# Kernel tuning notes

Measured on AMD Instinct MI355X. Metric: run time of the kernel, lower is better.

Reference implementation:

```python
import jax, jax.numpy as jnp
import numpy as np

N_NODES = 100000


def _add_self_loops(edges, n):
    loop = jnp.arange(n, dtype=edges.dtype)
    src = jnp.concatenate([edges[0], loop])
    dst = jnp.concatenate([edges[1], loop])
    return src, dst


def _gcn_conv(x, W, b, src, dst, dinv):
    # linear transform first (PyG GCNConv), then normalized scatter-add aggregation
    h = x @ W                                    # [N, out]
    norm = dinv[src] * dinv[dst]                 # [E]
    msg = h[src] * norm[:, None]                 # [E, out]
    out = jax.ops.segment_sum(msg, dst, num_segments=x.shape[0])
    return out + b


def setup_inputs() -> dict:
    key = jax.random.key(0)
    k1, k2, k3, k4 = jax.random.split(key, 4)
    feats, hidden, labels, n_edges = 128, 64, 16, 1600000
    features = jax.random.normal(k1, (N_NODES, feats), dtype=jnp.float32)
    edges = jax.random.randint(k2, (2, n_edges), 0, N_NODES, dtype=jnp.int64)
    W1 = jax.random.normal(k3, (feats, hidden), dtype=jnp.float32) * (1.0 / np.sqrt(feats))
    b1 = jnp.zeros((hidden,), dtype=jnp.float32)
    W2 = jax.random.normal(k4, (hidden, labels), dtype=jnp.float32) * (1.0 / np.sqrt(hidden))
    b2 = jnp.zeros((labels,), dtype=jnp.float32)
    return {"features": features, "edges": edges, "W1": W1, "b1": b1, "W2": W2, "b2": b2}


def reference(features, edges, W1, b1, W2, b2):
    n = features.shape[0]
    src, dst = _add_self_loops(edges, n)
    deg = jnp.zeros((n,), dtype=features.dtype).at[dst].add(1.0)  # in-degree incl. self loop
    dinv = jnp.where(deg > 0, jax.lax.rsqrt(deg), 0.0)
    h1 = jax.nn.relu(_gcn_conv(features, W1, b1, src, dst, dinv))
    h2 = _gcn_conv(h1, W2, b2, src, dst, dinv)
    return jax.nn.log_softmax(h2, axis=1)
```

## Files before the change

### kernel.cpp

```cpp
#include <hip/hip_runtime.h>
#include <math.h>

#define NN 100000
#define NE 1600000
#define FI 128
#define FH 64
#define FO 16
#define NB 392
#define BCAP 5632
#define AEPT 16
#define ACHUNK (256 * AEPT)
#define ABLK ((NE + ACHUNK - 1) / ACHUNK)
#define GBLK ((NN + 63) / 64)

typedef unsigned short ushort_t;
typedef __attribute__((ext_vector_type(8))) short bf16x8;
typedef __attribute__((ext_vector_type(4))) float f32x4;

__device__ __forceinline__ ushort_t f2bf(float f) {
    unsigned u = __float_as_uint(f);
    u = (u + 0x7fffu + ((u >> 16) & 1u)) >> 16;
    return (ushort_t)u;
}
__device__ __forceinline__ float bf_lo(unsigned u) {
    return __uint_as_float(u << 16);
}
__device__ __forceinline__ float bf_hi(unsigned u) {
    return __uint_as_float(u & 0xffff0000u);
}

__device__ __forceinline__ int load_dst(const int* edges, int mode, int e) {
    return mode ? edges[2 * (NE + e)] : edges[NE + e];
}
__device__ __forceinline__ int load_src(const int* edges, int mode, int e) {
    return mode ? edges[2 * e] : edges[e];
}

__global__ __launch_bounds__(256) void k_fuseA(const int* __restrict__ edges,
                                               unsigned* __restrict__ bcur,
                                               unsigned* __restrict__ staged,
                                               const float* __restrict__ x,
                                               const float* __restrict__ W1,
                                               ushort_t* __restrict__ h1p) {
    __shared__ unsigned pay_lds[ACHUNK];
    __shared__ ushort_t bkt_lds[ACHUNK];
    __shared__ unsigned hcnt[NB], hb[NB], dlt[NB], hcur[NB];
    __shared__ unsigned sc[512];
    __shared__ int smode;

    if (blockIdx.x >= ABLK) {
        const int tid = threadIdx.x;
        const int l = tid & 63;
        const int w = tid >> 6;
        const int m = l & 15;
        const int g = l >> 4;
        const int node0 = (blockIdx.x - ABLK) * 64 + w * 16;

        bf16x8 bfrag[4][4];
#pragma unroll
        for (int ks = 0; ks < 4; ++ks)
#pragma unroll
            for (int nt = 0; nt < 4; ++nt)
#pragma unroll
                for (int e = 0; e < 8; ++e)
                    bfrag[ks][nt][e] = (short)f2bf(W1[(ks * 32 + g * 8 + e) * FH + nt * 16 + m]);

        f32x4 acc[4];
#pragma unroll
        for (int nt = 0; nt < 4; ++nt) acc[nt] = (f32x4){0.f, 0.f, 0.f, 0.f};

        int node = node0 + m;
        const float* xrow = x + (size_t)(node < NN ? node : NN - 1) * FI;
#pragma unroll
        for (int ks = 0; ks < 4; ++ks) {
            float4 xa = *(const float4*)&xrow[ks * 32 + g * 8];
            float4 xb = *(const float4*)&xrow[ks * 32 + g * 8 + 4];
            bf16x8 afrag;
            afrag[0] = (short)f2bf(xa.x);
            afrag[1] = (short)f2bf(xa.y);
            afrag[2] = (short)f2bf(xa.z);
            afrag[3] = (short)f2bf(xa.w);
            afrag[4] = (short)f2bf(xb.x);
            afrag[5] = (short)f2bf(xb.y);
            afrag[6] = (short)f2bf(xb.z);
            afrag[7] = (short)f2bf(xb.w);
#pragma unroll
            for (int nt = 0; nt < 4; ++nt)
                acc[nt] = __builtin_amdgcn_mfma_f32_16x16x32_bf16(afrag, bfrag[ks][nt], acc[nt], 0, 0, 0);
        }
#pragma unroll
        for (int nt = 0; nt < 4; ++nt)
#pragma unroll
            for (int r = 0; r < 4; ++r) {
                int outnode = node0 + g * 4 + r;
                if (outnode < NN)
                    h1p[(size_t)outnode * FH + nt * 16 + m] = f2bf(acc[nt][r]);
            }
        return;
    }

    const int t = threadIdx.x;
    if (t == 0) {
        unsigned orv = 0;
        for (int i = 0; i < 16; ++i) orv |= (unsigned)edges[2 * i + 1];
        smode = (orv == 0u) ? 1 : 0;
    }
    for (int i = t; i < NB; i += 256) { hcnt[i] = 0; hcur[i] = 0; }
    __syncthreads();
    const int m = smode;
    const int base_e = blockIdx.x * ACHUNK;
    const int total = min(ACHUNK, NE - base_e);

    unsigned pay[AEPT];
    ushort_t bk[AEPT];
#pragma unroll
    for (int q = 0; q < AEPT; ++q) {
        int e = base_e + t + q * 256;
        pay[q] = 0;
        bk[q] = 0xffff;
        if (e < NE) {
            int d = load_dst(edges, m, e);
            int s = load_src(edges, m, e);
            pay[q] = ((unsigned)s << 8) | (unsigned)(d & 255);
            bk[q] = (ushort_t)(d >> 8);
            atomicAdd(&hcnt[d >> 8], 1u);
        }
    }
    __syncthreads();

    for (int i = t; i < NB; i += 256) dlt[i] = atomicAdd(&bcur[i], hcnt[i]);
    sc[t] = (t < NB) ? hcnt[t] : 0u;
    sc[t + 256] = (t + 256 < NB) ? hcnt[t + 256] : 0u;
    __syncthreads();
    for (int ofs = 1; ofs < 512; ofs <<= 1) {
        unsigned v0 = (t >= ofs) ? sc[t - ofs] : 0u;
        unsigned v1 = (t + 256 >= ofs) ? sc[t + 256 - ofs] : 0u;
        __syncthreads();
        sc[t] += v0;
        sc[t + 256] += v1;
        __syncthreads();
    }
    for (int i = t; i < NB; i += 256) hb[i] = sc[i] - hcnt[i];
    __syncthreads();
    for (int i = t; i < NB; i += 256) dlt[i] = dlt[i] - hb[i];
    __syncthreads();

#pragma unroll
    for (int q = 0; q < AEPT; ++q) {
        if (bk[q] != 0xffff) {
            unsigned b = bk[q];
            unsigned r = atomicAdd(&hcur[b], 1u);
            unsigned idx = hb[b] + r;
            pay_lds[idx] = pay[q];
            bkt_lds[idx] = (ushort_t)b;
        }
    }
    __syncthreads();

    for (int i = t; i < total; i += 256) {
        unsigned b = bkt_lds[i];
        unsigned within = (unsigned)i + dlt[b];
        if (within < BCAP)
            staged[(size_t)b * BCAP + within] = pay_lds[i];
    }
}

__global__ __launch_bounds__(256) void k_phaseB(const unsigned* __restrict__ staged,
                                                const unsigned* __restrict__ bcur,
                                                unsigned* __restrict__ rowstart,
                                                int* __restrict__ esrc,
                                                float* __restrict__ dinv) {
    __shared__ unsigned hist[256], hb[256], hcur[256], tmp[256];
    __shared__ unsigned sbc[512];
    const int b = blockIdx.x;
    const int t = threadIdx.x;

    sbc[t] = (t < NB) ? bcur[t] : 0u;
    sbc[t + 256] = (t + 256 < NB) ? bcur[t + 256] : 0u;
    __syncthreads();
    for (int ofs = 1; ofs < 512; ofs <<= 1) {
        unsigned v0 = (t >= ofs) ? sbc[t - ofs] : 0u;
        unsigned v1 = (t + 256 >= ofs) ? sbc[t + 256 - ofs] : 0u;
        __syncthreads();
        sbc[t] += v0;
        sbc[t + 256] += v1;
        __syncthreads();
    }
    const unsigned base = (b == 0) ? 0u : sbc[b - 1];
    const unsigned cnt = min(bcur[b], (unsigned)BCAP);

    hist[t] = 0;
    hcur[t] = 0;
    __syncthreads();
    const unsigned* sb = staged + (size_t)b * BCAP;
    for (unsigned i = t; i < cnt; i += 256) atomicAdd(&hist[sb[i] & 255u], 1u);
    __syncthreads();
    unsigned x = hist[t];
    tmp[t] = x;
    __syncthreads();
    for (int ofs = 1; ofs < 256; ofs <<= 1) {
        unsigned v = (t >= ofs) ? tmp[t - ofs] : 0u;
        __syncthreads();
        tmp[t] += v;
        __syncthreads();
    }
    hb[t] = tmp[t] - x;
    int v = b * 256 + t;
    if (v <= NN) rowstart[v] = base + hb[t];
    if (v < NN) dinv[v] = rsqrtf((float)(1u + x));
    __syncthreads();
    for (unsigned i = t; i < cnt; i += 256) {
        unsigned p = sb[i];
        unsigned dlo = p & 255u;
        unsigned pos = base + hb[dlo] + atomicAdd(&hcur[dlo], 1u);
        esrc[pos] = (int)(p >> 8);
    }
}

__global__ __launch_bounds__(256) void k_gather1f(const unsigned* __restrict__ rowstart,
                                                  const int* __restrict__ esrc,
                                                  const ushort_t* __restrict__ h1p,
                                                  const float* __restrict__ dinv,
                                                  const float* __restrict__ b1,
                                                  const float* __restrict__ W2,
                                                  ushort_t* __restrict__ h2p) {
    __shared__ float Ws2t[FO][FH];
    {
        int t = threadIdx.x;
#pragma unroll
        for (int i = 0; i < 4; ++i) {
            int q = t * 4 + i;
            int k = q >> 4, j = q & 15;
            Ws2t[j][k] = W2[q];
        }
    }
    __syncthreads();

    int wave = (blockIdx.x * 256 + threadIdx.x) >> 6;
    int lane = threadIdx.x & 63;
    int grp = lane >> 4;
    int fj = lane & 15;
    int v = wave * 4 + grp;
    if (v >= NN) return;

    const uint2* h2v = (const uint2*)h1p;
    unsigned beg = rowstart[v], end = rowstart[v + 1];
    float dv = dinv[v];
    float a0 = 0.f, a1 = 0.f, a2 = 0.f, a3 = 0.f;
    unsigned i = beg;
    int ns0 = 0, ns1 = 0, ns2 = 0, ns3 = 0;
    if (i + 3 < end) { ns0 = esrc[i]; ns1 = esrc[i + 1]; ns2 = esrc[i + 2]; ns3 = esrc[i + 3]; }
    while (i + 3 < end) {
        int s0 = ns0, s1 = ns1, s2 = ns2, s3 = ns3;
        unsigned nx = i + 4;
        if (nx + 3 < end) { ns0 = esrc[nx]; ns1 = esrc[nx + 1]; ns2 = esrc[nx + 2]; ns3 = esrc[nx + 3]; }
        float n0 = dinv[s0] * dv, n1 = dinv[s1] * dv;
        float n2 = dinv[s2] * dv, n3 = dinv[s3] * dv;
        uint2 u0 = h2v[(size_t)s0 * 16 + fj];
        uint2 u1 = h2v[(size_t)s1 * 16 + fj];
        uint2 u2 = h2v[(size_t)s2 * 16 + fj];
        uint2 u3 = h2v[(size_t)s3 * 16 + fj];
        a0 += bf_lo(u0.x) * n0 + bf_lo(u1.x) * n1 + bf_lo(u2.x) * n2 + bf_lo(u3.x) * n3;
        a1 += bf_hi(u0.x) * n0 + bf_hi(u1.x) * n1 + bf_hi(u2.x) * n2 + bf_hi(u3.x) * n3;
        a2 += bf_lo(u0.y) * n0 + bf_lo(u1.y) * n1 + bf_lo(u2.y) * n2 + bf_lo(u3.y) * n3;
        a3 += bf_hi(u0.y) * n0 + bf_hi(u1.y) * n1 + bf_hi(u2.y) * n2 + bf_hi(u3.y) * n3;
        i = nx;
    }
    for (; i < end; ++i) {
        int s = esrc[i];
        float n = dinv[s] * dv;
        uint2 u = h2v[(size_t)s * 16 + fj];
        a0 += bf_lo(u.x) * n;
        a1 += bf_hi(u.x) * n;
        a2 += bf_lo(u.y) * n;
        a3 += bf_hi(u.y) * n;
    }
    float di2 = dv * dv;
    uint2 us = h2v[(size_t)v * 16 + fj];
    float4 bb = ((const float4*)b1)[fj];
    float r0 = fmaxf(a0 + bf_lo(us.x) * di2 + bb.x, 0.f);
    float r1 = fmaxf(a1 + bf_hi(us.x) * di2 + bb.y, 0.f);
    float r2 = fmaxf(a2 + bf_lo(us.y) * di2 + bb.z, 0.f);
    float r3 = fmaxf(a3 + bf_hi(us.y) * di2 + bb.w, 0.f);

    float p[16];
#pragma unroll
    for (int j = 0; j < 16; ++j) {
        float4 w = *(const float4*)&Ws2t[j][fj * 4];
        p[j] = r0 * w.x + r1 * w.y + r2 * w.z + r3 * w.w;
    }
    bool c0 = (fj & 1) != 0;
    float q8[8];
#pragma unroll
    for (int k = 0; k < 8; ++k) {
        float sent = c0 ? p[2 * k] : p[2 * k + 1];
        float kept = c0 ? p[2 * k + 1] : p[2 * k];
        q8[k] = kept + __shfl_xor(sent, 1);
    }
    bool c1 = (fj & 2) != 0;
    float q4[4];
#pragma unroll
    for (int k = 0; k < 4; ++k) {
        float sent = c1 ? q8[2 * k] : q8[2 * k + 1];
        float kept = c1 ? q8[2 * k + 1] : q8[2 * k];
        q4[k] = kept + __shfl_xor(sent, 2);
    }
    bool c2 = (fj & 4) != 0;
    float q2[2];
#pragma unroll
    for (int k = 0; k < 2; ++k) {
        float sent = c2 ? q4[2 * k] : q4[2 * k + 1];
        float kept = c2 ? q4[2 * k + 1] : q4[2 * k];
        q2[k] = kept + __shfl_xor(sent, 4);
    }
    bool c3 = (fj & 8) != 0;
    {
        float sent = c3 ? q2[0] : q2[1];
        float kept = c3 ? q2[1] : q2[0];
        float fin = kept + __shfl_xor(sent, 8);
        h2p[(size_t)v * FO + fj] = f2bf(fin);
    }
}

__global__ __launch_bounds__(256) void k_gather2(const unsigned* __restrict__ rowstart,
                                                 const int* __restrict__ esrc,
                                                 const ushort_t* __restrict__ h2p,
                                                 const float* __restrict__ dinv,
                                                 const float* __restrict__ b,
                                                 float* __restrict__ out) {
    int wave = (blockIdx.x * 256 + threadIdx.x) >> 6;
    int lane = threadIdx.x & 63;
    int grp = lane >> 4;
    int j = lane & 15;
    int v = wave * 4 + grp;
    if (v >= NN) return;
    unsigned beg = rowstart[v], end = rowstart[v + 1];
    float dv = dinv[v];
    float acc = 0.f;
    unsigned i = beg;
    int ns0 = 0, ns1 = 0, ns2 = 0, ns3 = 0;
    if (i + 3 < end) { ns0 = esrc[i]; ns1 = esrc[i + 1]; ns2 = esrc[i + 2]; ns3 = esrc[i + 3]; }
    while (i + 3 < end) {
        int s0 = ns0, s1 = ns1, s2 = ns2, s3 = ns3;
        unsigned nx = i + 4;
        if (nx + 3 < end) { ns0 = esrc[nx]; ns1 = esrc[nx + 1]; ns2 = esrc[nx + 2]; ns3 = esrc[nx + 3]; }
        float n0 = dinv[s0] * dv, n1 = dinv[s1] * dv;
        float n2 = dinv[s2] * dv, n3 = dinv[s3] * dv;
        float x0 = __uint_as_float((unsigned)h2p[(size_t)s0 * FO + j] << 16);
        float x1 = __uint_as_float((unsigned)h2p[(size_t)s1 * FO + j] << 16);
        float x2 = __uint_as_float((unsigned)h2p[(size_t)s2 * FO + j] << 16);
        float x3 = __uint_as_float((unsigned)h2p[(size_t)s3 * FO + j] << 16);
        acc += x0 * n0 + x1 * n1 + x2 * n2 + x3 * n3;
        i = nx;
    }
    for (; i < end; ++i) {
        int s = esrc[i];
        acc += __uint_as_float((unsigned)h2p[(size_t)s * FO + j] << 16) * (dinv[s] * dv);
    }
    float val = acc + __uint_as_float((unsigned)h2p[(size_t)v * FO + j] << 16) * dv * dv + b[j];
    float m = val;
#pragma unroll
    for (int w = 1; w < 16; w <<= 1) m = fmaxf(m, __shfl_xor(m, w));
    float ex = expf(val - m);
    float ssum = ex;
#pragma unroll
    for (int w = 1; w < 16; w <<= 1) ssum += __shfl_xor(ssum, w);
    float res = val - (m + logf(ssum));
    out[(size_t)v * FO + j] = res;
}

extern "C" void kernel_launch(void* const* d_in, const int* in_sizes, int n_in,
                              void* d_out, int out_size, void* d_ws, size_t ws_size,
                              hipStream_t stream) {
    const float* x = (const float*)d_in[0];
    const int* edges = (const int*)d_in[1];
    const float* W1 = (const float*)d_in[2];
    const float* b1 = (const float*)d_in[3];
    const float* W2 = (const float*)d_in[4];
    const float* b2 = (const float*)d_in[5];
    float* out = (float*)d_out;

    char* ws = (char*)d_ws;
    size_t off = 0;
    auto take = [&](size_t bytes) {
        void* p = ws + off;
        off += (bytes + 255) & ~(size_t)255;
        return p;
    };
    unsigned* bcur = (unsigned*)take((size_t)NB * 4);
    unsigned* rowstart = (unsigned*)take((size_t)(NN + 1) * 4);
    float* dinv = (float*)take((size_t)NN * 4);
    int* esrc = (int*)take((size_t)NE * 4);
    ushort_t* h1p = (ushort_t*)take((size_t)NN * FH * 2);
    ushort_t* h2p = (ushort_t*)take((size_t)NN * FO * 2);
    unsigned* staged = (unsigned*)take((size_t)NB * BCAP * 4);

    hipMemsetAsync(bcur, 0, (size_t)NB * 4, stream);
    k_fuseA<<<ABLK + GBLK, 256, 0, stream>>>(edges, bcur, staged, x, W1, h1p);
    k_phaseB<<<NB, 256, 0, stream>>>(staged, bcur, rowstart, esrc, dinv);
    k_gather1f<<<(NN + 15) / 16, 256, 0, stream>>>(rowstart, esrc, h1p, dinv, b1, W2, h2p);
    k_gather2<<<(NN + 15) / 16, 256, 0, stream>>>(rowstart, esrc, h2p, dinv, b2, out);
}
```

Before: 113.9 us.

## Pre-scale node features by dinv to drop per-edge normalization gathers

Factors the symmetric normalization dinv[s]*dinv[d] so that source features are pre-multiplied by dinv[s]. For layer 1 this happens in a new pass at the end of phaseB that rescales h1 in place; for layer 2 the h2 output is scaled before it is stored. The aggregation loops then become plain sums followed by a single multiply by dinv[v], which removes the random dinv[s] gathers and the per-edge multiplies. The cost is an extra read-modify-write over h1 in phaseB and a second bf16 rounding of the scaled values.

```diff
diff --git a/kernel.cpp b/kernel.cpp
--- a/kernel.cpp
+++ b/kernel.cpp
@@ -169,7 +169,8 @@
                                                 const unsigned* __restrict__ bcur,
                                                 unsigned* __restrict__ rowstart,
                                                 int* __restrict__ esrc,
-                                                float* __restrict__ dinv) {
+                                                float* __restrict__ dinv,
+                                                ushort_t* __restrict__ h1p) {
     __shared__ unsigned hist[256], hb[256], hcur[256], tmp[256];
     __shared__ unsigned sbc[512];
     const int b = blockIdx.x;
@@ -206,14 +207,37 @@
     }
     hb[t] = tmp[t] - x;
     int v = b * 256 + t;
+    float dv = rsqrtf((float)(1u + x));
     if (v <= NN) rowstart[v] = base + hb[t];
-    if (v < NN) dinv[v] = rsqrtf((float)(1u + x));
+    if (v < NN) dinv[v] = dv;
     __syncthreads();
     for (unsigned i = t; i < cnt; i += 256) {
         unsigned p = sb[i];
         unsigned dlo = p & 255u;
         unsigned pos = base + hb[dlo] + atomicAdd(&hcur[dlo], 1u);
         esrc[pos] = (int)(p >> 8);
+    }
+
+    __syncthreads();
+    tmp[t] = __float_as_uint(dv);
+    __syncthreads();
+    unsigned* h32 = (unsigned*)h1p;
+    const int w = t >> 6;
+    const int lane = t & 63;
+    const int half = lane >> 5;
+    const int ui = lane & 31;
+#pragma unroll 4
+    for (int r2 = 0; r2 < 32; ++r2) {
+        int local = w * 64 + r2 * 2 + half;
+        int node = b * 256 + local;
+        if (node < NN) {
+            float dvr = __uint_as_float(tmp[local]);
+            size_t idx = (size_t)node * 32 + ui;
+            unsigned u = h32[idx];
+            float lo = bf_lo(u) * dvr;
+            float hi = bf_hi(u) * dvr;
+            h32[idx] = (unsigned)f2bf(lo) | ((unsigned)f2bf(hi) << 16);
+        }
     }
 }
 
@@ -254,34 +278,30 @@
         int s0 = ns0, s1 = ns1, s2 = ns2, s3 = ns3;
         unsigned nx = i + 4;
         if (nx + 3 < end) { ns0 = esrc[nx]; ns1 = esrc[nx + 1]; ns2 = esrc[nx + 2]; ns3 = esrc[nx + 3]; }
-        float n0 = dinv[s0] * dv, n1 = dinv[s1] * dv;
-        float n2 = dinv[s2] * dv, n3 = dinv[s3] * dv;
         uint2 u0 = h2v[(size_t)s0 * 16 + fj];
         uint2 u1 = h2v[(size_t)s1 * 16 + fj];
         uint2 u2 = h2v[(size_t)s2 * 16 + fj];
         uint2 u3 = h2v[(size_t)s3 * 16 + fj];
-        a0 += bf_lo(u0.x) * n0 + bf_lo(u1.x) * n1 + bf_lo(u2.x) * n2 + bf_lo(u3.x) * n3;
-        a1 += bf_hi(u0.x) * n0 + bf_hi(u1.x) * n1 + bf_hi(u2.x) * n2 + bf_hi(u3.x) * n3;
-        a2 += bf_lo(u0.y) * n0 + bf_lo(u1.y) * n1 + bf_lo(u2.y) * n2 + bf_lo(u3.y) * n3;
-        a3 += bf_hi(u0.y) * n0 + bf_hi(u1.y) * n1 + bf_hi(u2.y) * n2 + bf_hi(u3.y) * n3;
+        a0 += (bf_lo(u0.x) + bf_lo(u1.x)) + (bf_lo(u2.x) + bf_lo(u3.x));
+        a1 += (bf_hi(u0.x) + bf_hi(u1.x)) + (bf_hi(u2.x) + bf_hi(u3.x));
+        a2 += (bf_lo(u0.y) + bf_lo(u1.y)) + (bf_lo(u2.y) + bf_lo(u3.y));
+        a3 += (bf_hi(u0.y) + bf_hi(u1.y)) + (bf_hi(u2.y) + bf_hi(u3.y));
         i = nx;
     }
     for (; i < end; ++i) {
         int s = esrc[i];
-        float n = dinv[s] * dv;
         uint2 u = h2v[(size_t)s * 16 + fj];
-        a0 += bf_lo(u.x) * n;
-        a1 += bf_hi(u.x) * n;
-        a2 += bf_lo(u.y) * n;
-        a3 += bf_hi(u.y) * n;
-    }
-    float di2 = dv * dv;
+        a0 += bf_lo(u.x);
+        a1 += bf_hi(u.x);
+        a2 += bf_lo(u.y);
+        a3 += bf_hi(u.y);
+    }
     uint2 us = h2v[(size_t)v * 16 + fj];
     float4 bb = ((const float4*)b1)[fj];
-    float r0 = fmaxf(a0 + bf_lo(us.x) * di2 + bb.x, 0.f);
-    float r1 = fmaxf(a1 + bf_hi(us.x) * di2 + bb.y, 0.f);
-    float r2 = fmaxf(a2 + bf_lo(us.y) * di2 + bb.z, 0.f);
-    float r3 = fmaxf(a3 + bf_hi(us.y) * di2 + bb.w, 0.f);
+    float r0 = fmaxf(fmaf(a0 + bf_lo(us.x), dv, bb.x), 0.f);
+    float r1 = fmaxf(fmaf(a1 + bf_hi(us.x), dv, bb.y), 0.f);
+    float r2 = fmaxf(fmaf(a2 + bf_lo(us.y), dv, bb.z), 0.f);
+    float r3 = fmaxf(fmaf(a3 + bf_hi(us.y), dv, bb.w), 0.f);
 
     float p[16];
 #pragma unroll
@@ -318,7 +338,7 @@
         float sent = c3 ? q2[0] : q2[1];
         float kept = c3 ? q2[1] : q2[0];
         float fin = kept + __shfl_xor(sent, 8);
-        h2p[(size_t)v * FO + fj] = f2bf(fin);
+        h2p[(size_t)v * FO + fj] = f2bf(fin * dv);
     }
 }
 
@@ -344,20 +364,19 @@
         int s0 = ns0, s1 = ns1, s2 = ns2, s3 = ns3;
         unsigned nx = i + 4;
         if (nx + 3 < end) { ns0 = esrc[nx]; ns1 = esrc[nx + 1]; ns2 = esrc[nx + 2]; ns3 = esrc[nx + 3]; }
-        float n0 = dinv[s0] * dv, n1 = dinv[s1] * dv;
-        float n2 = dinv[s2] * dv, n3 = dinv[s3] * dv;
         float x0 = __uint_as_float((unsigned)h2p[(size_t)s0 * FO + j] << 16);
         float x1 = __uint_as_float((unsigned)h2p[(size_t)s1 * FO + j] << 16);
         float x2 = __uint_as_float((unsigned)h2p[(size_t)s2 * FO + j] << 16);
         float x3 = __uint_as_float((unsigned)h2p[(size_t)s3 * FO + j] << 16);
-        acc += x0 * n0 + x1 * n1 + x2 * n2 + x3 * n3;
+        acc += (x0 + x1) + (x2 + x3);
         i = nx;
     }
     for (; i < end; ++i) {
         int s = esrc[i];
-        acc += __uint_as_float((unsigned)h2p[(size_t)s * FO + j] << 16) * (dinv[s] * dv);
-    }
-    float val = acc + __uint_as_float((unsigned)h2p[(size_t)v * FO + j] << 16) * dv * dv + b[j];
+        acc += __uint_as_float((unsigned)h2p[(size_t)s * FO + j] << 16);
+    }
+    float self = __uint_as_float((unsigned)h2p[(size_t)v * FO + j] << 16);
+    float val = fmaf(acc + self, dv, b[j]);
     float m = val;
 #pragma unroll
     for (int w = 1; w < 16; w <<= 1) m = fmaxf(m, __shfl_xor(m, w));
@@ -397,7 +416,7 @@
 
     hipMemsetAsync(bcur, 0, (size_t)NB * 4, stream);
     k_fuseA<<<ABLK + GBLK, 256, 0, stream>>>(edges, bcur, staged, x, W1, h1p);
-    k_phaseB<<<NB, 256, 0, stream>>>(staged, bcur, rowstart, esrc, dinv);
+    k_phaseB<<<NB, 256, 0, stream>>>(staged, bcur, rowstart, esrc, dinv, h1p);
     k_gather1f<<<(NN + 15) / 16, 256, 0, stream>>>(rowstart, esrc, h1p, dinv, b1, W2, h2p);
     k_gather2<<<(NN + 15) / 16, 256, 0, stream>>>(rowstart, esrc, h2p, dinv, b2, out);
 }
```

Result: slower. 119.0 us (+4.5%).
